# Optimization experiments

Hardware: AMD Instinct MI355X
Metric: run time of the kernel (lower is better)

## Reference

```python
import jax, jax.numpy as jnp
import numpy as np


def setup_inputs() -> dict:
    key = jax.random.key(0)
    k1, k2, k3, k4, k5 = jax.random.split(key, 5)
    b, n, L, D, m = 8, 8192, 512, 128, 16
    x = jax.random.normal(k1, (b, n, L), dtype=jnp.float32)
    # attention MLP: Linear(L->D, no bias), Tanh, Linear(D->1, no bias)
    W1 = jax.random.normal(k2, (L, D), dtype=jnp.float32) / np.sqrt(L).astype(np.float32)
    W2 = jax.random.normal(k3, (D, 1), dtype=jnp.float32) / np.sqrt(D).astype(np.float32)
    batched_image_ids = jax.random.randint(k4, (b, n), 0, m)  # which image each packed token belongs to
    key_pad_mask = jax.random.bernoulli(k5, 0.1, (b, n))      # True = padding token
    return {"x": x, "W1": W1, "W2": W2,
            "batched_image_ids": batched_image_ids,
            "key_pad_mask": key_pad_mask,
            "max_queries": 16}


def reference(x, W1, W2, batched_image_ids, key_pad_mask, max_queries):
    # Attention scores per token: tanh(x W1) W2 -> [b, n, 1]
    A = jnp.tanh(x @ W1) @ W2
    A = jnp.swapaxes(A, -1, -2)  # [b, 1, n]
    b, n, d = x.shape
    # Per-image pooling mask: token j contributes to query i iff its image id == i and not padded
    image_id_arange = jnp.arange(max_queries)                                    # [m]
    attn_pool_mask = (image_id_arange[None, :, None] == batched_image_ids[:, None, :])
    attn_pool_mask = attn_pool_mask & (~key_pad_mask)[:, None, :]                # [b, m, n]
    neg = -jnp.finfo(A.dtype).max
    A = jnp.where(attn_pool_mask, jnp.broadcast_to(A, (b, max_queries, n)), neg)
    A = jax.nn.softmax(A, axis=-1)                                               # [b, m, n]
    out = jnp.einsum('bmn,bnd->bmd', A, x)                                       # pooled per image
    # num_images == max_queries for every bag -> is_images selects everything
    out = out.reshape(b * max_queries, d)
    return out
```

## Files before the change

kernel.cpp:

```cpp
#include <hip/hip_runtime.h>
#include <hip/hip_bf16.h>
#include <cstdint>
#include <cstddef>

typedef __attribute__((ext_vector_type(8))) short bf16x8;
typedef __attribute__((ext_vector_type(4))) float f32x4;

#define BATCH 8
#define NTOK 8192
#define LDIM 512
#define DDIM 128
#define NQ 16
#define NSEG 8
#define SEGLEN (NTOK / NSEG)

static __device__ __forceinline__ short f2bf(float f) {
  uint32_t u = __float_as_uint(f);
  uint32_t r = u + 0x7fffu + ((u >> 16) & 1u);
  return (short)(r >> 16);
}

static __device__ __forceinline__ bf16x8 cvt8(float4 a, float4 b) {
  bf16x8 o;
  o[0] = f2bf(a.x); o[1] = f2bf(a.y); o[2] = f2bf(a.z); o[3] = f2bf(a.w);
  o[4] = f2bf(b.x); o[5] = f2bf(b.y); o[6] = f2bf(b.z); o[7] = f2bf(b.w);
  return o;
}

static __device__ __forceinline__ bool is_pad(const void* pad, int byteFlag, int j) {
  return byteFlag ? (((const unsigned char*)pad)[j] != 0)
                  : (((const int*)pad)[j] != 0);
}

__global__ __launch_bounds__(256) void k0_wfrag(const float* __restrict__ W1,
                                                short* __restrict__ wfrag,
                                                const unsigned int* __restrict__ pad_raw,
                                                int* __restrict__ flag) {
  int tid = blockIdx.x * blockDim.x + threadIdx.x;
  if (tid < 16 * 8 * 64) {
    int l = tid & 63;
    int t = (tid >> 6) & 7;
    int c = tid >> 9;
    int kbase = c * 32 + (l >> 4) * 8;
    int col = t * 16 + (l & 15);
    bf16x8 frag;
#pragma unroll
    for (int i = 0; i < 8; ++i) frag[i] = f2bf(W1[(size_t)(kbase + i) * DDIM + col]);
    ((bf16x8*)wfrag)[tid] = frag;
  }
  if (blockIdx.x == 0) {
    int any_gt1 = 0;
    for (int i = threadIdx.x; i < 16384; i += 256)
      if (pad_raw[i] > 1u) any_gt1 = 1;
    unsigned long long m = __ballot(any_gt1);
    __shared__ int s[4];
    if ((threadIdx.x & 63) == 0) s[threadIdx.x >> 6] = (m != 0ull) ? 1 : 0;
    __syncthreads();
    if (threadIdx.x == 0) flag[0] = (s[0] | s[1] | s[2] | s[3]);
  }
}

__global__ __launch_bounds__(512, 6) void k1_scores(const float* __restrict__ x,
                                                    const short* __restrict__ wfrag,
                                                    const float* __restrict__ W2,
                                                    float* __restrict__ expw) {
  __shared__ short ldsw[16384];
  const int tid = threadIdx.x, wave = tid >> 6, lane = tid & 63;
  const int rowBase = blockIdx.x * 128 + wave * 16;
  const float* xp = x + (size_t)(rowBase + (lane & 15)) * LDIM + ((lane >> 4) * 8);

#define STAGE(qd)                                                                             \
  {                                                                                           \
    const unsigned int* src_ = (const unsigned int*)wfrag + (qd) * 8192;                      \
    _Pragma("unroll")                                                                         \
    for (int i = 0; i < 4; ++i) {                                                             \
      __builtin_amdgcn_global_load_lds(                                                       \
          (const __attribute__((address_space(1))) unsigned int*)(src_ + (i * 512 + tid) * 4),\
          (__attribute__((address_space(3))) unsigned int*)&ldsw[(i * 512 + wave * 64) * 8],  \
          16, 0, 0);                                                                          \
    }                                                                                         \
  }

#define ALOAD(dst, c)                                  \
  {                                                    \
    dst[0] = *(const float4*)(xp + (c) * 32);          \
    dst[1] = *(const float4*)(xp + (c) * 32 + 4);      \
  }

  f32x4 acc[8];
#pragma unroll
  for (int t = 0; t < 8; ++t) acc[t] = (f32x4){0.f, 0.f, 0.f, 0.f};
  float4 avbuf[4][2];

  STAGE(0);
  ALOAD(avbuf[0], 0);
  ALOAD(avbuf[1], 1);
  ALOAD(avbuf[2], 2);
  ALOAD(avbuf[3], 3);
  __syncthreads();

#pragma unroll
  for (int qd = 0; qd < 4; ++qd) {
#pragma unroll
    for (int cc = 0; cc < 4; ++cc) {
      const int c = qd * 4 + cc;
      bf16x8 af = cvt8(avbuf[c & 3][0], avbuf[c & 3][1]);
      if (c < 12) ALOAD(avbuf[c & 3], c + 4);
#pragma unroll
      for (int t = 0; t < 8; ++t) {
        bf16x8 bfr = *(const bf16x8*)&ldsw[((cc * 8 + t) * 64 + lane) * 8];
        acc[t] = __builtin_amdgcn_mfma_f32_16x16x32_bf16(af, bfr, acc[t], 0, 0, 0);
      }
    }
    if (qd < 3) {
      __syncthreads();
      STAGE(qd + 1);
      __syncthreads();
    }
  }
#undef STAGE
#undef ALOAD

  float w2v[8];
#pragma unroll
  for (int t = 0; t < 8; ++t) w2v[t] = W2[t * 16 + (lane & 15)];
  float asum[4] = {0.f, 0.f, 0.f, 0.f};
#pragma unroll
  for (int t = 0; t < 8; ++t) {
#pragma unroll
    for (int r = 0; r < 4; ++r) {
      float h = 1.f - 2.f / (__expf(2.f * acc[t][r]) + 1.f);
      asum[r] += h * w2v[t];
    }
  }
#pragma unroll
  for (int m = 1; m < 16; m <<= 1) {
#pragma unroll
    for (int r = 0; r < 4; ++r) asum[r] += __shfl_xor(asum[r], m, 64);
  }
  if ((lane & 15) == 0) {
    int rb = rowBase + (lane >> 4) * 4;
#pragma unroll
    for (int r = 0; r < 4; ++r) expw[rb + r] = __expf(asum[r]);
  }
}

__global__ __launch_bounds__(512) void k3_pool(const float* __restrict__ x,
                                               const float* __restrict__ expw,
                                               const int* __restrict__ ids,
                                               const void* __restrict__ pad,
                                               const int* __restrict__ flag,
                                               float* __restrict__ partial,
                                               float* __restrict__ wsum) {
  int blk = blockIdx.x;
  int s = blk & 7, q = (blk >> 3) & 15, b = blk >> 7;
  int wave = threadIdx.x >> 6, lane = threadIdx.x & 63;
  int bfl = flag[0];
  __shared__ float w_u[1024];
  __shared__ unsigned short j_u[1024];
  __shared__ int cnt[8];
  __shared__ float wred[8];

  const int base = b * NTOK;
  const int tokBase = s * SEGLEN + wave * 128;

  int myCnt = 0;
#pragma unroll
  for (int g = 0; g < 2; ++g) {
    int j = tokBase + g * 64 + lane;
    bool mem = (ids[base + j] == q) && !is_pad(pad, bfl, base + j);
    myCnt += __popcll(__ballot(mem));
  }
  if (lane == 0) cnt[wave] = myCnt;
  __syncthreads();

  int wpos = 0;
#pragma unroll
  for (int w = 0; w < 8; ++w) if (w < wave) wpos += cnt[w];
  const int total = cnt[0] + cnt[1] + cnt[2] + cnt[3] + cnt[4] + cnt[5] + cnt[6] + cnt[7];

  float wacc = 0.f;
#pragma unroll
  for (int g = 0; g < 2; ++g) {
    int j = tokBase + g * 64 + lane;
    bool mem = (ids[base + j] == q) && !is_pad(pad, bfl, base + j);
    float wt = mem ? expw[base + j] : 0.f;
    wacc += wt;
    unsigned long long mask = __ballot(mem);
    if (mem) {
      int pos = wpos + __popcll(mask & ((1ull << lane) - 1ull));
      w_u[pos] = wt;
      j_u[pos] = (unsigned short)j;
    }
    wpos += __popcll(mask);
  }
#pragma unroll
  for (int m = 1; m < 64; m <<= 1) wacc += __shfl_xor(wacc, m, 64);
  if (lane == 0) wred[wave] = wacc;
  __syncthreads();

  int grp = threadIdx.x >> 7, ct = threadIdx.x & 127;
  int c0 = ct * 4;
  int per = (total + 3) >> 2;
  int e0 = grp * per;
  int e1 = e0 + per; if (e1 > total) e1 = total;
  float4 av = {0.f, 0.f, 0.f, 0.f};
  if (e0 < e1) {
    float4 cur = *(const float4*)(x + (size_t)(base + j_u[e0]) * LDIM + c0);
    int e = e0;
    for (; e + 1 < e1; ++e) {
      float4 nxt = *(const float4*)(x + (size_t)(base + j_u[e + 1]) * LDIM + c0);
      float wt = w_u[e];
      av.x = fmaf(wt, cur.x, av.x); av.y = fmaf(wt, cur.y, av.y);
      av.z = fmaf(wt, cur.z, av.z); av.w = fmaf(wt, cur.w, av.w);
      cur = nxt;
    }
    float wt = w_u[e];
    av.x = fmaf(wt, cur.x, av.x); av.y = fmaf(wt, cur.y, av.y);
    av.z = fmaf(wt, cur.z, av.z); av.w = fmaf(wt, cur.w, av.w);
  }
  *(float4*)(partial + ((size_t)(blk * 4 + grp)) * LDIM + c0) = av;
  if (threadIdx.x == 0)
    wsum[blk] = wred[0] + wred[1] + wred[2] + wred[3] + wred[4] + wred[5] + wred[6] + wred[7];
}

__global__ __launch_bounds__(512) void k4_reduce(const float* __restrict__ partial,
                                                 const float* __restrict__ wsum,
                                                 float* __restrict__ out) {
  int bq = blockIdx.x;
  int b = bq >> 4, q = bq & 15;
  int c = threadIdx.x;
  float ws = 0.f;
#pragma unroll
  for (int s = 0; s < 8; ++s) ws += wsum[b * 128 + q * 8 + s];
  float ps = 0.f;
#pragma unroll
  for (int s = 0; s < 8; ++s)
#pragma unroll
    for (int g = 0; g < 4; ++g)
      ps += partial[((size_t)((b * 128 + q * 8 + s) * 4 + g)) * LDIM + c];
  out[bq * 512 + c] = (ws > 0.f) ? (ps / ws) : 0.f;
}

extern "C" void kernel_launch(void* const* d_in, const int* in_sizes, int n_in,
                              void* d_out, int out_size, void* d_ws, size_t ws_size,
                              hipStream_t stream) {
  const float* x = (const float*)d_in[0];
  const float* W1 = (const float*)d_in[1];
  const float* W2 = (const float*)d_in[2];
  const int* ids = (const int*)d_in[3];
  const void* pad = d_in[4];
  float* out = (float*)d_out;

  char* ws = (char*)d_ws;
  short* wfrag = (short*)ws;
  int* flag = (int*)(ws + 131072);
  float* expw = (float*)(ws + 131200);
  float* wsum = (float*)(ws + 393344);
  float* partial = (float*)(ws + 397440);

  hipLaunchKernelGGL(k0_wfrag, dim3(32), dim3(256), 0, stream,
                     W1, wfrag, (const unsigned int*)pad, flag);
  hipLaunchKernelGGL(k1_scores, dim3((BATCH * NTOK) / 128), dim3(512), 0, stream,
                     x, wfrag, W2, expw);
  hipLaunchKernelGGL(k3_pool, dim3(BATCH * NQ * NSEG), dim3(512), 0, stream,
                     x, expw, ids, pad, flag, partial, wsum);
  hipLaunchKernelGGL(k4_reduce, dim3(BATCH * NQ), dim3(512), 0, stream,
                     partial, wsum, out);
}
```

Before: 66.58 us.

## Write bf16 copy of x in score kernel and pool from it

The score kernel now stores the bf16-converted x tiles it already builds for the MFMA to a workspace buffer. The pooling kernel gathers these half-width rows instead of fp32 x, halving the bytes of its gather traffic. Pooling segments are doubled to 16 and the reduce kernel is split into two column halves, so there are more, smaller blocks. bf16 conversion now uses packed hardware convert instructions. The trade-off is an extra 64 MB write in the score kernel and reduced precision of pooled values.

```diff
diff --git a/kernel.cpp b/kernel.cpp
--- a/kernel.cpp
+++ b/kernel.cpp
@@ -11,7 +11,7 @@
 #define LDIM 512
 #define DDIM 128
 #define NQ 16
-#define NSEG 8
+#define NSEG 16
 #define SEGLEN (NTOK / NSEG)
 
 static __device__ __forceinline__ short f2bf(float f) {
@@ -21,10 +21,16 @@
 }
 
 static __device__ __forceinline__ bf16x8 cvt8(float4 a, float4 b) {
-  bf16x8 o;
-  o[0] = f2bf(a.x); o[1] = f2bf(a.y); o[2] = f2bf(a.z); o[3] = f2bf(a.w);
-  o[4] = f2bf(b.x); o[5] = f2bf(b.y); o[6] = f2bf(b.z); o[7] = f2bf(b.w);
-  return o;
+  union { uint32_t u[4]; bf16x8 v; } r;
+  asm("v_cvt_pk_bf16_f32 %0, %1, %2" : "=v"(r.u[0]) : "v"(a.x), "v"(a.y));
+  asm("v_cvt_pk_bf16_f32 %0, %1, %2" : "=v"(r.u[1]) : "v"(a.z), "v"(a.w));
+  asm("v_cvt_pk_bf16_f32 %0, %1, %2" : "=v"(r.u[2]) : "v"(b.x), "v"(b.y));
+  asm("v_cvt_pk_bf16_f32 %0, %1, %2" : "=v"(r.u[3]) : "v"(b.z), "v"(b.w));
+  return r.v;
+}
+
+static __device__ __forceinline__ float bf2f(unsigned short u) {
+  return __uint_as_float(((uint32_t)u) << 16);
 }
 
 static __device__ __forceinline__ bool is_pad(const void* pad, int byteFlag, int j) {
@@ -60,14 +66,18 @@
   }
 }
 
-__global__ __launch_bounds__(512, 6) void k1_scores(const float* __restrict__ x,
+__global__ __launch_bounds__(512, 4) void k1_scores(const float* __restrict__ x,
                                                     const short* __restrict__ wfrag,
                                                     const float* __restrict__ W2,
-                                                    float* __restrict__ expw) {
+                                                    float* __restrict__ expw,
+                                                    short* __restrict__ x_bf) {
   __shared__ short ldsw[16384];
   const int tid = threadIdx.x, wave = tid >> 6, lane = tid & 63;
+  const int g = lane >> 4;
   const int rowBase = blockIdx.x * 128 + wave * 16;
-  const float* xp = x + (size_t)(rowBase + (lane & 15)) * LDIM + ((lane >> 4) * 8);
+  const size_t rowOff = (size_t)(rowBase + (lane & 15)) * LDIM + g * 8;
+  const float* xp = x + rowOff;
+  short* xbp = x_bf + rowOff;
 
 #define STAGE(qd)                                                                             \
   {                                                                                           \
@@ -105,6 +115,7 @@
     for (int cc = 0; cc < 4; ++cc) {
       const int c = qd * 4 + cc;
       bf16x8 af = cvt8(avbuf[c & 3][0], avbuf[c & 3][1]);
+      *(bf16x8*)(xbp + c * 32) = af;
       if (c < 12) ALOAD(avbuf[c & 3], c + 4);
 #pragma unroll
       for (int t = 0; t < 8; ++t) {
@@ -145,7 +156,7 @@
   }
 }
 
-__global__ __launch_bounds__(512) void k3_pool(const float* __restrict__ x,
+__global__ __launch_bounds__(512) void k3_pool(const short* __restrict__ x_bf,
                                                const float* __restrict__ expw,
                                                const int* __restrict__ ids,
                                                const void* __restrict__ pad,
@@ -153,25 +164,22 @@
                                                float* __restrict__ partial,
                                                float* __restrict__ wsum) {
   int blk = blockIdx.x;
-  int s = blk & 7, q = (blk >> 3) & 15, b = blk >> 7;
+  int s = blk & 15, q = (blk >> 4) & 15, b = blk >> 8;
   int wave = threadIdx.x >> 6, lane = threadIdx.x & 63;
   int bfl = flag[0];
-  __shared__ float w_u[1024];
-  __shared__ unsigned short j_u[1024];
+  __shared__ float w_u[512];
+  __shared__ unsigned short j_u[512];
   __shared__ int cnt[8];
   __shared__ float wred[8];
 
   const int base = b * NTOK;
-  const int tokBase = s * SEGLEN + wave * 128;
-
-  int myCnt = 0;
-#pragma unroll
-  for (int g = 0; g < 2; ++g) {
-    int j = tokBase + g * 64 + lane;
-    bool mem = (ids[base + j] == q) && !is_pad(pad, bfl, base + j);
-    myCnt += __popcll(__ballot(mem));
-  }
-  if (lane == 0) cnt[wave] = myCnt;
+  const int j = s * SEGLEN + wave * 64 + lane;
+
+  bool mem = (ids[base + j] == q) && !is_pad(pad, bfl, base + j);
+  float wt = mem ? expw[base + j] : 0.f;
+  unsigned long long m0 = __ballot(mem);
+  int cw = __popcll(m0);
+  if (lane == 0) cnt[wave] = cw;
   __syncthreads();
 
   int wpos = 0;
@@ -179,21 +187,12 @@
   for (int w = 0; w < 8; ++w) if (w < wave) wpos += cnt[w];
   const int total = cnt[0] + cnt[1] + cnt[2] + cnt[3] + cnt[4] + cnt[5] + cnt[6] + cnt[7];
 
-  float wacc = 0.f;
-#pragma unroll
-  for (int g = 0; g < 2; ++g) {
-    int j = tokBase + g * 64 + lane;
-    bool mem = (ids[base + j] == q) && !is_pad(pad, bfl, base + j);
-    float wt = mem ? expw[base + j] : 0.f;
-    wacc += wt;
-    unsigned long long mask = __ballot(mem);
-    if (mem) {
-      int pos = wpos + __popcll(mask & ((1ull << lane) - 1ull));
-      w_u[pos] = wt;
-      j_u[pos] = (unsigned short)j;
-    }
-    wpos += __popcll(mask);
-  }
+  if (mem) {
+    int pos = wpos + __popcll(m0 & ((1ull << lane) - 1ull));
+    w_u[pos] = wt;
+    j_u[pos] = (unsigned short)j;
+  }
+  float wacc = wt;
 #pragma unroll
   for (int m = 1; m < 64; m <<= 1) wacc += __shfl_xor(wacc, m, 64);
   if (lane == 0) wred[wave] = wacc;
@@ -206,39 +205,39 @@
   int e1 = e0 + per; if (e1 > total) e1 = total;
   float4 av = {0.f, 0.f, 0.f, 0.f};
   if (e0 < e1) {
-    float4 cur = *(const float4*)(x + (size_t)(base + j_u[e0]) * LDIM + c0);
+    ushort4 cur = *(const ushort4*)(x_bf + (size_t)(base + j_u[e0]) * LDIM + c0);
     int e = e0;
     for (; e + 1 < e1; ++e) {
-      float4 nxt = *(const float4*)(x + (size_t)(base + j_u[e + 1]) * LDIM + c0);
-      float wt = w_u[e];
-      av.x = fmaf(wt, cur.x, av.x); av.y = fmaf(wt, cur.y, av.y);
-      av.z = fmaf(wt, cur.z, av.z); av.w = fmaf(wt, cur.w, av.w);
+      ushort4 nxt = *(const ushort4*)(x_bf + (size_t)(base + j_u[e + 1]) * LDIM + c0);
+      float w = w_u[e];
+      av.x = fmaf(w, bf2f(cur.x), av.x); av.y = fmaf(w, bf2f(cur.y), av.y);
+      av.z = fmaf(w, bf2f(cur.z), av.z); av.w = fmaf(w, bf2f(cur.w), av.w);
       cur = nxt;
     }
-    float wt = w_u[e];
-    av.x = fmaf(wt, cur.x, av.x); av.y = fmaf(wt, cur.y, av.y);
-    av.z = fmaf(wt, cur.z, av.z); av.w = fmaf(wt, cur.w, av.w);
+    float w = w_u[e];
+    av.x = fmaf(w, bf2f(cur.x), av.x); av.y = fmaf(w, bf2f(cur.y), av.y);
+    av.z = fmaf(w, bf2f(cur.z), av.z); av.w = fmaf(w, bf2f(cur.w), av.w);
   }
   *(float4*)(partial + ((size_t)(blk * 4 + grp)) * LDIM + c0) = av;
   if (threadIdx.x == 0)
     wsum[blk] = wred[0] + wred[1] + wred[2] + wred[3] + wred[4] + wred[5] + wred[6] + wred[7];
 }
 
-__global__ __launch_bounds__(512) void k4_reduce(const float* __restrict__ partial,
+__global__ __launch_bounds__(256) void k4_reduce(const float* __restrict__ partial,
                                                  const float* __restrict__ wsum,
                                                  float* __restrict__ out) {
-  int bq = blockIdx.x;
-  int b = bq >> 4, q = bq & 15;
-  int c = threadIdx.x;
+  int half = blockIdx.x & 1;
+  int bq = blockIdx.x >> 1;
+  int c = half * 256 + threadIdx.x;
   float ws = 0.f;
 #pragma unroll
-  for (int s = 0; s < 8; ++s) ws += wsum[b * 128 + q * 8 + s];
+  for (int s = 0; s < 16; ++s) ws += wsum[bq * 16 + s];
   float ps = 0.f;
 #pragma unroll
-  for (int s = 0; s < 8; ++s)
+  for (int s = 0; s < 16; ++s)
 #pragma unroll
     for (int g = 0; g < 4; ++g)
-      ps += partial[((size_t)((b * 128 + q * 8 + s) * 4 + g)) * LDIM + c];
+      ps += partial[((size_t)((bq * 16 + s) * 4 + g)) * LDIM + c];
   out[bq * 512 + c] = (ws > 0.f) ? (ps / ws) : 0.f;
 }
 
@@ -257,14 +256,15 @@
   int* flag = (int*)(ws + 131072);
   float* expw = (float*)(ws + 131200);
   float* wsum = (float*)(ws + 393344);
-  float* partial = (float*)(ws + 397440);
+  float* partial = (float*)(ws + 401536);
+  short* x_bf = (short*)(ws + 17178752);
 
   hipLaunchKernelGGL(k0_wfrag, dim3(32), dim3(256), 0, stream,
                      W1, wfrag, (const unsigned int*)pad, flag);
   hipLaunchKernelGGL(k1_scores, dim3((BATCH * NTOK) / 128), dim3(512), 0, stream,
-                     x, wfrag, W2, expw);
+                     x, wfrag, W2, expw, x_bf);
   hipLaunchKernelGGL(k3_pool, dim3(BATCH * NQ * NSEG), dim3(512), 0, stream,
-                     x, expw, ids, pad, flag, partial, wsum);
-  hipLaunchKernelGGL(k4_reduce, dim3(BATCH * NQ), dim3(512), 0, stream,
+                     x_bf, expw, ids, pad, flag, partial, wsum);
+  hipLaunchKernelGGL(k4_reduce, dim3(BATCH * NQ * 2), dim3(256), 0, stream,
                      partial, wsum, out);
 }
```

After: 70.57 us. 1.06x slower.
